# Kernel tuning notes

Measured on AMD Instinct MI355X. Metric: run time of the kernel, lower is better.

The kernel has to match this reference:

```python
import jax, jax.numpy as jnp
import numpy as np


def setup_inputs() -> dict:
    key = jax.random.key(0)
    k1, k2 = jax.random.split(key)
    B, C, H, W = 4, 256, 64, 64
    f_m = jax.random.normal(k1, (B, C, H, W), dtype=jnp.float32)
    f_d = jax.random.normal(k2, (B, C, H, W), dtype=jnp.float32)
    return {"f_m": f_m, "f_d": f_d}


def reference(f_m, f_d):
    B, C, H, W = f_d.shape
    HW = H * W
    f_fuse = f_m + f_d                      # [B, C, H, W]
    f_c = f_fuse.reshape(B, C, HW)          # [B, C, HW]
    # scores[b, n, m] = sum_c f_c[b, c, n] * f_c[b, c, m]
    scores = jnp.einsum('bcn,bcm->bnm', f_c, f_c)   # [B, HW, HW]
    att = jax.nn.softmax(scores, axis=-1)           # softmax over last dim
    f_d_r = f_d.reshape(B, C, HW)                   # [B, C, HW]
    # out[b, c, m] = sum_n f_d_r[b, c, n] * att[b, n, m]
    f_d_att = jnp.einsum('bcn,bnm->bcm', f_d_r, att).reshape(B, C, H, W)
    return f_d_att + f_d
```

## Files before the change

kernel.cpp:

```cpp
#include <hip/hip_runtime.h>
#include <math.h>

#define B_ 4
#define C_ 256
#define N_ 4096
#define LDE 68
#define LDX 72

typedef __attribute__((ext_vector_type(8))) short short8;
typedef __attribute__((ext_vector_type(4))) float f32x4;
typedef __attribute__((ext_vector_type(2))) float f32x2;
typedef __attribute__((ext_vector_type(2))) long long2v;

__device__ inline ushort f2bf(float f) {
    uint u = __float_as_uint(f);
    return (ushort)((u + 0x7fffu + ((u >> 16) & 1u)) >> 16);
}
__device__ inline float bf2f(ushort h) { return __uint_as_float(((uint)h) << 16); }

__device__ inline f32x4 mfma16(short8 a, short8 b, f32x4 c) {
    return __builtin_amdgcn_mfma_f32_16x16x32_bf16(a, b, c, 0, 0, 0);
}
__device__ inline f32x4 mfma8(long a, long b, f32x4 c) {
    return __builtin_amdgcn_mfma_f32_16x16x32_fp8_fp8(a, b, c, 0, 0, 0);
}

__device__ inline size_t xfi16(int b, int nt, int kk2) {
    return (((size_t)(b * 256 + nt)) * 4 + kk2) * 1024;
}
__device__ inline size_t xfi8(int b, int nt, int kk) {
    return (((size_t)(b * 256 + nt)) * 8 + kk) * 512;
}
__device__ inline size_t ffi(int b, int nc, int ct, int k2) {
    return ((((size_t)(b * 64 + nc)) * 16 + ct) * 2 + k2) * 512;
}
__device__ inline size_t eti(int b, int mt, int ng) {
    return (((size_t)(b * 256 + mt)) * 512 + (size_t)ng) * 128;
}
__device__ inline size_t zmi(int b, int nc, int mt) {
    return ((size_t)(b * 64 + nc)) * 256 + mt;
}

__global__ __launch_bounds__(256) void prep_x_kernel(const float* __restrict__ fm,
                                                     const float* __restrict__ fd,
                                                     uchar* __restrict__ xfrag8) {
    __shared__ ushort xl[64][LDX];
    const int b = blockIdx.z, c0 = blockIdx.y * 64, n0 = blockIdx.x * 64;
    const int t = threadIdx.x;
    const int n4 = (t & 15) * 4, cl = t >> 4;
    const size_t base = (size_t)b * C_ * N_;
    #pragma unroll
    for (int p = 0; p < 4; ++p) {
        const int cr = 16 * p + cl;
        const float4 m4 = *(const float4*)(fm + base + (size_t)(c0 + cr) * N_ + n0 + n4);
        const float4 d4 = *(const float4*)(fd + base + (size_t)(c0 + cr) * N_ + n0 + n4);
        ushort4 xo;
        xo.x = f2bf(m4.x + d4.x); xo.y = f2bf(m4.y + d4.y);
        xo.z = f2bf(m4.z + d4.z); xo.w = f2bf(m4.w + d4.w);
        *(ushort4*)(&xl[cr][n4]) = xo;
    }
    __syncthreads();
    const int l = t & 63, tl = t >> 6;
    const int nl = 16 * tl + (l & 15);
    uint dd[4];
    #pragma unroll
    for (int j = 0; j < 2; ++j) {
        const int cb = 32 * j + 8 * (l >> 4);
        float f[8];
        #pragma unroll
        for (int i = 0; i < 8; ++i) f[i] = bf2f(xl[cb + i][nl]);
        int d0 = __builtin_amdgcn_cvt_pk_fp8_f32(f[0], f[1], 0, 0);
        d0 = __builtin_amdgcn_cvt_pk_fp8_f32(f[2], f[3], d0, 1);
        int d1 = __builtin_amdgcn_cvt_pk_fp8_f32(f[4], f[5], 0, 0);
        d1 = __builtin_amdgcn_cvt_pk_fp8_f32(f[6], f[7], d1, 1);
        dd[2 * j] = (uint)d0; dd[2 * j + 1] = (uint)d1;
    }
    uint* dst = (uint*)(xfrag8 + xfi16(b, (n0 >> 4) + tl, c0 >> 6) + (size_t)l * 16);
    dst[0] = dd[0]; dst[1] = dd[1]; dst[2] = dd[2]; dst[3] = dd[3];
}

__global__ __launch_bounds__(256) void dg_kernel(const uchar* __restrict__ xfrag8,
                                                 float* __restrict__ dgall,
                                                 float* __restrict__ rsadd,
                                                 uchar* __restrict__ zmask) {
    const int t = threadIdx.x, lane = t & 63, w = t >> 6;
    const int tid = blockIdx.x * 4 + w;
    const int b = tid >> 8, nt = tid & 255;
    const int l15 = lane & 15, q = lane >> 4;
    long2v af[4];
    #pragma unroll
    for (int kk2 = 0; kk2 < 4; ++kk2)
        af[kk2] = *(const long2v*)(xfrag8 + xfi16(b, nt, kk2) + (size_t)lane * 16);
    f32x4 dacc = {0.f, 0.f, 0.f, 0.f};
    #pragma unroll
    for (int kk2 = 0; kk2 < 4; ++kk2) {
        dacc = mfma8(af[kk2].x, af[kk2].x, dacc);
        dacc = mfma8(af[kk2].y, af[kk2].y, dacc);
    }
    float dvv[4];
    #pragma unroll
    for (int r = 0; r < 4; ++r)
        dvv[r] = __shfl(dacc[r], 20 * q + r, 64);
    if (l15 == 0) {
        #pragma unroll
        for (int r = 0; r < 4; ++r)
            dgall[b * N_ + 16 * nt + 4 * q + r] = dvv[r];
    }
    const int zi = blockIdx.x * 256 + t;
    if (zi < B_ * N_) rsadd[zi] = 0.f;
    zmask[zi] = 0;
}

__global__ __launch_bounds__(512, 2) void lsum_t_kernel(const uchar* __restrict__ xfrag8,
                                                        const float* __restrict__ dgall,
                                                        uchar* __restrict__ E8,
                                                        uchar* __restrict__ zmask,
                                                        float* __restrict__ rsbase,
                                                        float* __restrict__ rsadd) {
    __shared__ float red[8][64];
    __shared__ uchar chl[34];
    __shared__ int cnt_s;
    __shared__ uint zst[34];
    const int bid = blockIdx.x;
    const int b = (bid >> 1) & 3;
    const int n0 = ((((bid >> 3) << 1) | (bid & 1))) * 64;
    const int j = n0 >> 6;
    const int t = threadIdx.x, lane = t & 63, w = t >> 6;
    const int l15 = lane & 15, q = lane >> 4;
    const int g = w >> 2, wm = w & 3;

    if (t == 0) {
        int c = 0;
        chl[c++] = (uchar)j;
        for (int k = 0; k < 64; ++k) {
            if (k == j) continue;
            const bool own = (k > j) ? (((j + k) & 1) == 0) : (((j + k) & 1) == 1);
            if (own) chl[c++] = (uchar)k;
        }
        cnt_s = c;
    }
    if (t < 34) zst[t] = 0u;

    long2v af[4][4];
    #pragma unroll
    for (int ns = 0; ns < 4; ++ns)
        #pragma unroll
        for (int kk2 = 0; kk2 < 4; ++kk2)
            af[ns][kk2] = *(const long2v*)(xfrag8 + xfi16(b, (n0 >> 4) + ns, kk2) + (size_t)lane * 16);

    float dv[4][4];
    #pragma unroll
    for (int ns = 0; ns < 4; ++ns)
        #pragma unroll
        for (int r = 0; r < 4; ++r)
            dv[ns][r] = dgall[b * N_ + n0 + 16 * ns + 4 * q + r];
    float dvmin = dv[0][0];
    #pragma unroll
    for (int ns = 0; ns < 4; ++ns)
        #pragma unroll
        for (int r = 0; r < 4; ++r)
            dvmin = fminf(dvmin, dv[ns][r]);

    __syncthreads();
    const int cnt = cnt_s;

    long2v bn[4];
    float dgm_cur;
    {
        const int mt0 = 4 * (int)chl[g] + wm;
        #pragma unroll
        for (int kk2 = 0; kk2 < 4; ++kk2)
            bn[kk2] = *(const long2v*)(xfrag8 + xfi16(b, mt0, kk2) + (size_t)lane * 16);
        dgm_cur = dgall[b * N_ + 16 * mt0 + l15];
    }
    const size_t ebl = (size_t)l15 * 8 + 4 * (q & 1);
    const int ngb = (n0 >> 3) + (q >> 1);

    float rs[4][4] = {};
    for (int it = 0; it < 17; ++it) {
        const int idx = 2 * it + g;
        const bool valid = idx < cnt;
        const int kc = chl[valid ? idx : 0];
        const int mt = 4 * kc + wm;
        int idxn = 2 * (it + 1) + g; if (idxn >= cnt) idxn = 0;
        const int mtn = 4 * (int)chl[idxn] + wm;

        f32x4 a0 = {0.f,0.f,0.f,0.f}, a1 = {0.f,0.f,0.f,0.f};
        f32x4 a2 = {0.f,0.f,0.f,0.f}, a3 = {0.f,0.f,0.f,0.f};
        __builtin_amdgcn_s_setprio(1);
        #pragma unroll
        for (int kk2 = 0; kk2 < 4; ++kk2) {
            const long2v bc = bn[kk2];
            a0 = mfma8(af[0][kk2].x, bc.x, a0);
            a1 = mfma8(af[1][kk2].x, bc.x, a1);
            a2 = mfma8(af[2][kk2].x, bc.x, a2);
            a3 = mfma8(af[3][kk2].x, bc.x, a3);
            a0 = mfma8(af[0][kk2].y, bc.y, a0);
            a1 = mfma8(af[1][kk2].y, bc.y, a1);
            a2 = mfma8(af[2][kk2].y, bc.y, a2);
            a3 = mfma8(af[3][kk2].y, bc.y, a3);
            bn[kk2] = *(const long2v*)(xfrag8 + xfi16(b, mtn, kk2) + (size_t)lane * 16);
        }
        __builtin_amdgcn_s_setprio(0);
        const float dgm = dgm_cur;
        dgm_cur = dgall[b * N_ + 16 * mtn + l15];

        const float gmax = fmaxf(
            fmaxf(fmaxf(fmaxf(a0[0], a0[1]), fmaxf(a0[2], a0[3])),
                  fmaxf(fmaxf(a1[0], a1[1]), fmaxf(a1[2], a1[3]))),
            fmaxf(fmaxf(fmaxf(a2[0], a2[1]), fmaxf(a2[2], a2[3])),
                  fmaxf(fmaxf(a3[0], a3[1]), fmaxf(a3[2], a3[3]))));
        const bool hot = valid && (__ballot(gmax - fminf(dvmin, dgm) > -30.0f) != 0ULL);
        if (!hot) continue;

        float df[4][4];
#define EDF(AA, NS)                                                    \
        df[NS][0] = AA[0] - dv[NS][0]; df[NS][1] = AA[1] - dv[NS][1];  \
        df[NS][2] = AA[2] - dv[NS][2]; df[NS][3] = AA[3] - dv[NS][3];
        EDF(a0, 0) EDF(a1, 1) EDF(a2, 2) EDF(a3, 3)
#undef EDF
        const float mxA = fmaxf(
            fmaxf(fmaxf(fmaxf(df[0][0], df[0][1]), fmaxf(df[0][2], df[0][3])),
                  fmaxf(fmaxf(df[1][0], df[1][1]), fmaxf(df[1][2], df[1][3]))),
            fmaxf(fmaxf(fmaxf(df[2][0], df[2][1]), fmaxf(df[2][2], df[2][3])),
                  fmaxf(fmaxf(df[3][0], df[3][1]), fmaxf(df[3][2], df[3][3]))));
        const bool nzA = (__ballot(mxA > -30.0f) != 0ULL);
        if (nzA) {
            if (lane == 0) zmask[zmi(b, j, mt)] = 1;
            uint dpk[4];
#define EEXP(NS)                                                                       \
            {                                                                          \
                float e0 = __expf(df[NS][0]), e1 = __expf(df[NS][1]);                  \
                float e2 = __expf(df[NS][2]), e3 = __expf(df[NS][3]);                  \
                rs[NS][0] += e0; rs[NS][1] += e1; rs[NS][2] += e2; rs[NS][3] += e3;    \
                int d = __builtin_amdgcn_cvt_pk_fp8_f32(e0, e1, 0, 0);                 \
                d = __builtin_amdgcn_cvt_pk_fp8_f32(e2, e3, d, 1);                     \
                dpk[NS] = (uint)d;                                                     \
            }
            EEXP(0) EEXP(1) EEXP(2) EEXP(3)
#undef EEXP
            #pragma unroll
            for (int ns = 0; ns < 4; ++ns)
                *(uint*)(E8 + eti(b, mt, ngb + 2 * ns) + ebl) = dpk[ns];
        }
        if (kc != j) {
            float dfB[4][4];
            #pragma unroll
            for (int ns = 0; ns < 4; ++ns) {
                dfB[ns][0] = (ns==0?a0[0]:ns==1?a1[0]:ns==2?a2[0]:a3[0]) - dgm;
                dfB[ns][1] = (ns==0?a0[1]:ns==1?a1[1]:ns==2?a2[1]:a3[1]) - dgm;
                dfB[ns][2] = (ns==0?a0[2]:ns==1?a1[2]:ns==2?a2[2]:a3[2]) - dgm;
                dfB[ns][3] = (ns==0?a0[3]:ns==1?a1[3]:ns==2?a2[3]:a3[3]) - dgm;
            }
            uint bits = 0;
            #pragma unroll
            for (int ns = 0; ns < 4; ++ns) {
                const float m2 = fmaxf(fmaxf(dfB[ns][0], dfB[ns][1]),
                                       fmaxf(dfB[ns][2], dfB[ns][3]));
                if (__ballot(m2 > -30.0f) != 0ULL) bits |= (1u << ns);
            }
            if (bits) {
                if (lane == 0) atomicOr(&zst[idx], bits);
                float cs = 0.f;
                #pragma unroll
                for (int ns = 0; ns < 4; ++ns)
                    #pragma unroll
                    for (int r = 0; r < 4; ++r)
                        cs += __expf(dfB[ns][r]);
                cs += __shfl_xor(cs, 16, 64);
                cs += __shfl_xor(cs, 32, 64);
                if (q == 0) atomicAdd(rsadd + b * N_ + 16 * mt + l15, cs);
            }
        }
    }
    #pragma unroll
    for (int off = 1; off < 16; off <<= 1)
        #pragma unroll
        for (int ns = 0; ns < 4; ++ns)
            #pragma unroll
            for (int r = 0; r < 4; ++r)
                rs[ns][r] += __shfl_xor(rs[ns][r], off, 64);
    if (l15 == 0) {
        #pragma unroll
        for (int ns = 0; ns < 4; ++ns)
            #pragma unroll
            for (int r = 0; r < 4; ++r)
                red[w][16 * ns + 4 * q + r] = rs[ns][r];
    }
    __syncthreads();
    if (t < 64) {
        float s = 0.f;
        #pragma unroll
        for (int ww = 0; ww < 8; ++ww) s += red[ww][t];
        rsbase[b * N_ + n0 + t] = s;
    }
    if (t >= 64 && t < 64 + 33 * 4) {
        const int ii = (t - 64) >> 2, ns = (t - 64) & 3;
        const int idx = ii + 1;
        if (idx < cnt) {
            const int kc = chl[idx];
            if ((zst[idx] >> ns) & 1u) zmask[zmi(b, kc, 4 * j + ns)] = 2;
        }
    }
}

__global__ __launch_bounds__(512, 2) void out_e_kernel(const uchar* __restrict__ E8,
                                                       const uchar* __restrict__ zmask,
                                                       const float* __restrict__ rsbase,
                                                       const float* __restrict__ rsadd,
                                                       const float* __restrict__ dgall,
                                                       const uchar* __restrict__ xfrag8,
                                                       const float* __restrict__ fd32,
                                                       float* __restrict__ outp) {
    __shared__ ushort esc[8][16][66];
    const int bid = blockIdx.x;
    const int b = (bid >> 1) & 3;
    const int m0 = ((((bid >> 3) << 1) | (bid & 1))) * 64;
    const int t = threadIdx.x, lane = t & 63, w = t >> 6;
    const int l15 = lane & 15, q = lane >> 4;
    const size_t fb = (size_t)b * C_ * N_;
    const uchar* mrow = zmask + zmi(b, 0, m0 >> 4);

    f32x4 acc[2][4];
    #pragma unroll
    for (int ct = 0; ct < 2; ++ct)
        #pragma unroll
        for (int mt = 0; mt < 4; ++mt)
            acc[ct][mt] = (f32x4){0.f, 0.f, 0.f, 0.f};

    for (int gg = 0; gg < 8; ++gg) {
        uint mk[8];
        #pragma unroll
        for (int i = 0; i < 8; ++i)
            mk[i] = *(const uint*)(mrow + (size_t)(8 * gg + i) * 256);
        #pragma unroll
        for (int i = 0; i < 8; ++i) {
            const uint mki = mk[i];
            if (mki == 0) continue;
            const int nc = 8 * gg + i;
            const float* rb = rsbase + b * N_ + 64 * nc + 8 * q;
            const float* ra = rsadd + b * N_ + 64 * nc + 8 * q;
            float4 s0[2], s1[2];
            #pragma unroll
            for (int k2 = 0; k2 < 2; ++k2) {
                const float4 b0 = *(const float4*)(rb + 32 * k2);
                const float4 b1 = *(const float4*)(rb + 32 * k2 + 4);
                const float4 a0v = *(const float4*)(ra + 32 * k2);
                const float4 a1v = *(const float4*)(ra + 32 * k2 + 4);
                s0[k2].x = 1.0f / (b0.x + a0v.x); s0[k2].y = 1.0f / (b0.y + a0v.y);
                s0[k2].z = 1.0f / (b0.z + a0v.z); s0[k2].w = 1.0f / (b0.w + a0v.w);
                s1[k2].x = 1.0f / (b1.x + a1v.x); s1[k2].y = 1.0f / (b1.y + a1v.y);
                s1[k2].z = 1.0f / (b1.z + a1v.z); s1[k2].w = 1.0f / (b1.w + a1v.w);
            }
            short8 fn[2][2];
            #pragma unroll
            for (int ct = 0; ct < 2; ++ct) {
                const int c = 32 * w + 16 * ct + l15;
                const float* frow = fd32 + fb + (size_t)c * N_ + 64 * nc + 8 * q;
                #pragma unroll
                for (int k2 = 0; k2 < 2; ++k2) {
                    const float4 fa = *(const float4*)(frow + 32 * k2);
                    const float4 fb4 = *(const float4*)(frow + 32 * k2 + 4);
                    union { ushort us[8]; short8 v; } u;
                    u.us[0] = f2bf(fa.x * s0[k2].x); u.us[1] = f2bf(fa.y * s0[k2].y);
                    u.us[2] = f2bf(fa.z * s0[k2].z); u.us[3] = f2bf(fa.w * s0[k2].w);
                    u.us[4] = f2bf(fb4.x * s1[k2].x); u.us[5] = f2bf(fb4.y * s1[k2].y);
                    u.us[6] = f2bf(fb4.z * s1[k2].z); u.us[7] = f2bf(fb4.w * s1[k2].w);
                    fn[ct][k2] = u.v;
                }
            }
            if ((mki & ~0x01010101u) == 0u) {
                #pragma unroll
                for (int k2 = 0; k2 < 2; ++k2) {
                    #pragma unroll
                    for (int mt = 0; mt < 4; ++mt) {
                        if (((mki >> (8 * mt)) & 0xffu) != 1u) continue;
                        const long e8 = *(const long*)(E8 + eti(b, (m0 >> 4) + mt, 8 * nc + 4 * k2 + q) + (size_t)l15 * 8);
                        const uint lo = (uint)(unsigned long)e8;
                        const uint hi = (uint)((unsigned long)e8 >> 32);
                        const f32x2 f01 = __builtin_amdgcn_cvt_pk_f32_fp8((int)lo, false);
                        const f32x2 f23 = __builtin_amdgcn_cvt_pk_f32_fp8((int)lo, true);
                        const f32x2 f45 = __builtin_amdgcn_cvt_pk_f32_fp8((int)hi, false);
                        const f32x2 f67 = __builtin_amdgcn_cvt_pk_f32_fp8((int)hi, true);
                        union { uint u[4]; short8 v; } be;
                        asm("v_cvt_pk_bf16_f32 %0, %1, %2" : "=v"(be.u[0]) : "v"(f01.x), "v"(f01.y));
                        asm("v_cvt_pk_bf16_f32 %0, %1, %2" : "=v"(be.u[1]) : "v"(f23.x), "v"(f23.y));
                        asm("v_cvt_pk_bf16_f32 %0, %1, %2" : "=v"(be.u[2]) : "v"(f45.x), "v"(f45.y));
                        asm("v_cvt_pk_bf16_f32 %0, %1, %2" : "=v"(be.u[3]) : "v"(f67.x), "v"(f67.y));
                        acc[0][mt] = mfma16(fn[0][k2], be.v, acc[0][mt]);
                        acc[1][mt] = mfma16(fn[1][k2], be.v, acc[1][mt]);
                    }
                }
            } else {
                #pragma unroll
                for (int mt = 0; mt < 4; ++mt) {
                    long2v bmf[4];
                    #pragma unroll
                    for (int kk2 = 0; kk2 < 4; ++kk2)
                        bmf[kk2] = *(const long2v*)(xfrag8 + xfi16(b, (m0 >> 4) + mt, kk2) + (size_t)lane * 16);
                    #pragma unroll
                    for (int nt = 0; nt < 4; ++nt) {
                        long2v anf[4];
                        #pragma unroll
                        for (int kk2 = 0; kk2 < 4; ++kk2)
                            anf[kk2] = *(const long2v*)(xfrag8 + xfi16(b, 4 * nc + nt, kk2) + (size_t)lane * 16);
                        f32x4 sacc = {0.f, 0.f, 0.f, 0.f};
                        #pragma unroll
                        for (int kk2 = 0; kk2 < 4; ++kk2) {
                            sacc = mfma8(anf[kk2].x, bmf[kk2].x, sacc);
                            sacc = mfma8(anf[kk2].y, bmf[kk2].y, sacc);
                        }
                        #pragma unroll
                        for (int r = 0; r < 4; ++r) {
                            const float gv = dgall[b * N_ + 64 * nc + 16 * nt + 4 * q + r];
                            esc[w][l15][16 * nt + 4 * q + r] = f2bf(__expf(sacc[r] - gv));
                        }
                    }
                    #pragma unroll
                    for (int k2 = 0; k2 < 2; ++k2) {
                        const short8 be = *(const short8*)(&esc[w][l15][32 * k2 + 8 * q]);
                        acc[0][mt] = mfma16(fn[0][k2], be, acc[0][mt]);
                        acc[1][mt] = mfma16(fn[1][k2], be, acc[1][mt]);
                    }
                }
            }
        }
    }
    #pragma unroll
    for (int ct = 0; ct < 2; ++ct)
        #pragma unroll
        for (int mt = 0; mt < 4; ++mt)
            #pragma unroll
            for (int r = 0; r < 4; ++r) {
                const int c = 32 * w + 16 * ct + 4 * q + r;
                const int m = m0 + 16 * mt + l15;
                const size_t o = fb + (size_t)c * N_ + m;
                outp[o] = acc[ct][mt][r] + fd32[o];
            }
}

__global__ __launch_bounds__(256) void prep_kernel(const float* __restrict__ fm,
                                                   const float* __restrict__ fd,
                                                   uchar* __restrict__ xfrag8,
                                                   ushort* __restrict__ ffrag) {
    __shared__ ushort xl[64][LDX];
    __shared__ ushort fl[64][LDX];
    const int b = blockIdx.z, c0 = blockIdx.y * 64, n0 = blockIdx.x * 64;
    const int t = threadIdx.x;
    const int n4 = (t & 15) * 4, cl = t >> 4;
    const size_t base = (size_t)b * C_ * N_;
    #pragma unroll
    for (int p = 0; p < 4; ++p) {
        const int cr = 16 * p + cl;
        const float4 m4 = *(const float4*)(fm + base + (size_t)(c0 + cr) * N_ + n0 + n4);
        const float4 d4 = *(const float4*)(fd + base + (size_t)(c0 + cr) * N_ + n0 + n4);
        ushort4 fo;
        fo.x = f2bf(d4.x); fo.y = f2bf(d4.y); fo.z = f2bf(d4.z); fo.w = f2bf(d4.w);
        *(ushort4*)(&fl[cr][n4]) = fo;
        ushort4 xo;
        xo.x = f2bf(m4.x + d4.x); xo.y = f2bf(m4.y + d4.y);
        xo.z = f2bf(m4.z + d4.z); xo.w = f2bf(m4.w + d4.w);
        *(ushort4*)(&xl[cr][n4]) = xo;
    }
    __syncthreads();
    const int l = t & 63, tl = t >> 6;
    {
        const int nl = 16 * tl + (l & 15);
        #pragma unroll
        for (int j = 0; j < 2; ++j) {
            const int kk = (c0 >> 5) + j;
            const int cb = 32 * j + 8 * (l >> 4);
            float f[8];
            #pragma unroll
            for (int i = 0; i < 8; ++i) f[i] = bf2f(xl[cb + i][nl]);
            int d0 = __builtin_amdgcn_cvt_pk_fp8_f32(f[0], f[1], 0, 0);
            d0 = __builtin_amdgcn_cvt_pk_fp8_f32(f[2], f[3], d0, 1);
            int d1 = __builtin_amdgcn_cvt_pk_fp8_f32(f[4], f[5], 0, 0);
            d1 = __builtin_amdgcn_cvt_pk_fp8_f32(f[6], f[7], d1, 1);
            uint* dst = (uint*)(xfrag8 + xfi8(b, (n0 >> 4) + tl, kk) + (size_t)l * 8);
            dst[0] = (uint)d0; dst[1] = (uint)d1;
        }
    }
    {
        const int row = 16 * tl + (l & 15);
        #pragma unroll
        for (int k2 = 0; k2 < 2; ++k2) {
            const int col = 32 * k2 + 8 * (l >> 4);
            const ushort4 a0 = *(const ushort4*)(&fl[row][col]);
            const ushort4 a1 = *(const ushort4*)(&fl[row][col + 4]);
            ushort* dst = ffrag + ffi(b, n0 >> 6, (c0 >> 4) + tl, k2) + l * 8;
            *(ushort4*)(dst) = a0; *(ushort4*)(dst + 4) = a1;
        }
    }
}

__global__ __launch_bounds__(512, 2) void lsum_g_kernel(const uchar* __restrict__ xfrag8,
                                                        float* __restrict__ lg) {
    __shared__ float red[8][64];
    __shared__ float dgl[64];
    const int bid = blockIdx.x;
    const int b = (bid >> 1) & 3;
    const int n0 = ((((bid >> 3) << 1) | (bid & 1))) * 64;
    const int t = threadIdx.x, lane = t & 63, w = t >> 6;
    const int l15 = lane & 15, q = lane >> 4;

    long af[4][8];
    #pragma unroll
    for (int ns = 0; ns < 4; ++ns)
        #pragma unroll
        for (int kk = 0; kk < 8; ++kk)
            af[ns][kk] = *(const long*)(xfrag8 + xfi8(b, (n0 >> 4) + ns, kk) + (size_t)lane * 8);

    float dv[4][4];
    #pragma unroll
    for (int ns = 0; ns < 4; ++ns) {
        f32x4 dacc = {0.f, 0.f, 0.f, 0.f};
        #pragma unroll
        for (int kk = 0; kk < 8; ++kk)
            dacc = mfma8(af[ns][kk], af[ns][kk], dacc);
        #pragma unroll
        for (int r = 0; r < 4; ++r)
            dv[ns][r] = __shfl(dacc[r], 20 * q + r, 64);
    }
    if (w == 0 && l15 == 0) {
        #pragma unroll
        for (int ns = 0; ns < 4; ++ns)
            #pragma unroll
            for (int r = 0; r < 4; ++r)
                dgl[16 * ns + 4 * q + r] = dv[ns][r];
    }

    long bn[8];
    #pragma unroll
    for (int kk = 0; kk < 8; ++kk)
        bn[kk] = *(const long*)(xfrag8 + xfi8(b, w, kk) + (size_t)lane * 8);

    float rs[4][4] = {};
    for (int mc = 0; mc < 32; ++mc) {
        const int mtn = (mc + 1 < 32) ? (mc + 1) * 8 + w : w;
        f32x4 a0 = {0.f,0.f,0.f,0.f}, a1 = {0.f,0.f,0.f,0.f};
        f32x4 a2 = {0.f,0.f,0.f,0.f}, a3 = {0.f,0.f,0.f,0.f};
        #pragma unroll
        for (int kk = 0; kk < 8; ++kk) {
            const long bc = bn[kk];
            a0 = mfma8(af[0][kk], bc, a0);
            a1 = mfma8(af[1][kk], bc, a1);
            a2 = mfma8(af[2][kk], bc, a2);
            a3 = mfma8(af[3][kk], bc, a3);
            bn[kk] = *(const long*)(xfrag8 + xfi8(b, mtn, kk) + (size_t)lane * 8);
        }
        #pragma unroll
        for (int r = 0; r < 4; ++r) {
            rs[0][r] += __expf(a0[r] - dv[0][r]);
            rs[1][r] += __expf(a1[r] - dv[1][r]);
            rs[2][r] += __expf(a2[r] - dv[2][r]);
            rs[3][r] += __expf(a3[r] - dv[3][r]);
        }
    }
    #pragma unroll
    for (int off = 1; off < 16; off <<= 1)
        #pragma unroll
        for (int ns = 0; ns < 4; ++ns)
            #pragma unroll
            for (int r = 0; r < 4; ++r)
                rs[ns][r] += __shfl_xor(rs[ns][r], off, 64);
    if (l15 == 0) {
        #pragma unroll
        for (int ns = 0; ns < 4; ++ns)
            #pragma unroll
            for (int r = 0; r < 4; ++r)
                red[w][16 * ns + 4 * q + r] = rs[ns][r];
    }
    __syncthreads();
    if (t < 64) {
        float s = 0.f;
        #pragma unroll
        for (int ww = 0; ww < 8; ++ww) s += red[ww][t];
        lg[b * N_ + n0 + t] = dgl[t] + __logf(s);
    }
}

__global__ __launch_bounds__(512, 2) void out_g_kernel(const uchar* __restrict__ xfrag8,
                                                       const ushort* __restrict__ ffrag,
                                                       const float* __restrict__ gg,
                                                       const float* __restrict__ fd32,
                                                       float* __restrict__ outp) {
    __shared__ ushort ET[2][64][LDE];
    const int bid = blockIdx.x;
    const int b = (bid >> 1) & 3;
    const int m0 = ((((bid >> 3) << 1) | (bid & 1))) * 64;
    const int t = threadIdx.x, lane = t & 63, w = t >> 6;
    const int l15 = lane & 15, q = lane >> 4;
    const int a = w & 3, h = w >> 2;
    const size_t fb = (size_t)b * C_ * N_;

    long bfr[2][8];
    #pragma unroll
    for (int jt = 0; jt < 2; ++jt)
        #pragma unroll
        for (int kk = 0; kk < 8; ++kk)
            bfr[jt][kk] = *(const long*)(xfrag8 + xfi8(b, (m0 >> 4) + 2 * h + jt, kk) + (size_t)lane * 8);

    f32x4 acc[2][4];
    #pragma unroll
    for (int ct = 0; ct < 2; ++ct)
        #pragma unroll
        for (int mt = 0; mt < 4; ++mt)
            acc[ct][mt] = (f32x4){0.f, 0.f, 0.f, 0.f};

    long an[8];
    #pragma unroll
    for (int kk = 0; kk < 8; ++kk)
        an[kk] = *(const long*)(xfrag8 + xfi8(b, a, kk) + (size_t)lane * 8);
    float gn[4];
    #pragma unroll
    for (int r = 0; r < 4; ++r) gn[r] = gg[b * N_ + 16 * a + 4 * q + r];

    int p = 0;
    for (int n0c = 0; n0c < N_; n0c += 64, p ^= 1) {
        const int nc = n0c >> 6;
        short8 fn[2][2];
        #pragma unroll
        for (int ct = 0; ct < 2; ++ct)
            #pragma unroll
            for (int k2 = 0; k2 < 2; ++k2)
                fn[ct][k2] = *(const short8*)(ffrag + ffi(b, nc, 2 * w + ct, k2) + lane * 8);
        float gv[4];
        #pragma unroll
        for (int r = 0; r < 4; ++r) gv[r] = gn[r];
        const int nx = (n0c + 64 < N_) ? n0c + 64 : 0;
        #pragma unroll
        for (int r = 0; r < 4; ++r) gn[r] = gg[b * N_ + nx + 16 * a + 4 * q + r];

        f32x4 s0 = {0.f, 0.f, 0.f, 0.f}, s1 = {0.f, 0.f, 0.f, 0.f};
        #pragma unroll
        for (int kk = 0; kk < 8; ++kk) {
            s0 = mfma8(an[kk], bfr[0][kk], s0);
            s1 = mfma8(an[kk], bfr[1][kk], s1);
            an[kk] = *(const long*)(xfrag8 + xfi8(b, (nx >> 4) + a, kk) + (size_t)lane * 8);
        }
        ushort4 e0, e1;
        e0.x = f2bf(__expf(s0[0] - gv[0])); e0.y = f2bf(__expf(s0[1] - gv[1]));
        e0.z = f2bf(__expf(s0[2] - gv[2])); e0.w = f2bf(__expf(s0[3] - gv[3]));
        e1.x = f2bf(__expf(s1[0] - gv[0])); e1.y = f2bf(__expf(s1[1] - gv[1]));
        e1.z = f2bf(__expf(s1[2] - gv[2])); e1.w = f2bf(__expf(s1[3] - gv[3]));
        *(ushort4*)(&ET[p][32 * h + l15][16 * a + 4 * q])      = e0;
        *(ushort4*)(&ET[p][32 * h + 16 + l15][16 * a + 4 * q]) = e1;

        asm volatile("s_waitcnt lgkmcnt(0)\n\ts_barrier" ::: "memory");

        #pragma unroll
        for (int k2 = 0; k2 < 2; ++k2) {
            #pragma unroll
            for (int mt = 0; mt < 4; ++mt) {
                const short8 be = *(const short8*)(&ET[p][16 * mt + l15][32 * k2 + 8 * q]);
                acc[0][mt] = mfma16(fn[0][k2], be, acc[0][mt]);
                acc[1][mt] = mfma16(fn[1][k2], be, acc[1][mt]);
            }
        }
    }
    #pragma unroll
    for (int ct = 0; ct < 2; ++ct)
        #pragma unroll
        for (int mt = 0; mt < 4; ++mt)
            #pragma unroll
            for (int r = 0; r < 4; ++r) {
                const int c = 32 * w + 16 * ct + 4 * q + r;
                const int m = m0 + 16 * mt + l15;
                const size_t o = fb + (size_t)c * N_ + m;
                outp[o] = acc[ct][mt][r] + fd32[o];
            }
}

extern "C" void kernel_launch(void* const* d_in, const int* in_sizes, int n_in,
                              void* d_out, int out_size, void* d_ws, size_t ws_size,
                              hipStream_t stream) {
    const float* fm = (const float*)d_in[0];
    const float* fd = (const float*)d_in[1];
    float* outp = (float*)d_out;

    const size_t xb_elts = (size_t)B_ * N_ * C_;
    const size_t e_bytes = (size_t)B_ * N_ * N_;
    const size_t z_bytes = (size_t)B_ * 64 * 256;
    const size_t f_bytes = (size_t)B_ * N_ * 4;
    const size_t need_e  = xb_elts + e_bytes + z_bytes + 3 * f_bytes;
    const size_t need_g  = xb_elts * 3 + f_bytes;

    uchar* xfrag8 = (uchar*)d_ws;

    if (ws_size >= need_e) {
        uchar* E8     = xfrag8 + xb_elts;
        uchar* zmask  = E8 + e_bytes;
        float* rsbase = (float*)(zmask + z_bytes);
        float* rsadd  = rsbase + (size_t)B_ * N_;
        float* dgall  = rsadd + (size_t)B_ * N_;
        prep_x_kernel<<<dim3(N_ / 64, C_ / 64, B_), 256, 0, stream>>>(fm, fd, xfrag8);
        dg_kernel<<<dim3(256), 256, 0, stream>>>(xfrag8, dgall, rsadd, zmask);
        lsum_t_kernel<<<dim3(256), 512, 0, stream>>>(xfrag8, dgall, E8, zmask, rsbase, rsadd);
        out_e_kernel<<<dim3(256), 512, 0, stream>>>(E8, zmask, rsbase, rsadd, dgall, xfrag8, fd, outp);
    } else if (ws_size >= need_g) {
        ushort* ffrag = (ushort*)(xfrag8 + xb_elts);
        float*  lg    = (float*)(xfrag8 + xb_elts * 3);
        prep_kernel<<<dim3(N_ / 64, C_ / 64, B_), 256, 0, stream>>>(fm, fd, xfrag8, ffrag);
        lsum_g_kernel<<<dim3(256), 512, 0, stream>>>(xfrag8, lg);
        out_g_kernel<<<dim3(256), 512, 0, stream>>>(xfrag8, ffrag, lg, fd, outp);
    }
}
```

Measured before the change: 109.1 us.

## Fuse diagonal-block output into row-sum kernel and skip clean output blocks

The row-sum kernel now keeps the diagonal attention tile in shared memory as bf16 and, once the row sums are known, computes that block's output contribution directly (f_d scaled by the inverse row sum, times the diagonal exp tile) and writes out = acc + f_d. The second kernel first checks the zmask for any off-diagonal nonzero tiles or cross-block flags and returns early when the diagonal alone is enough. This targets the common case where the input's strong self-similarity makes the softmax essentially diagonal, avoiding the full E8 output pass. It adds shared memory and work to the first kernel, and relies on out_fix correctly recomputing and overwriting blocks that need off-diagonal terms.

```diff
diff --git a/kernel.cpp b/kernel.cpp
--- a/kernel.cpp
+++ b/kernel.cpp
@@ -111,13 +111,17 @@
     zmask[zi] = 0;
 }
 
-__global__ __launch_bounds__(512, 2) void lsum_t_kernel(const uchar* __restrict__ xfrag8,
-                                                        const float* __restrict__ dgall,
-                                                        uchar* __restrict__ E8,
-                                                        uchar* __restrict__ zmask,
-                                                        float* __restrict__ rsbase,
-                                                        float* __restrict__ rsadd) {
+__global__ __launch_bounds__(512, 2) void fused_kernel(const uchar* __restrict__ xfrag8,
+                                                       const float* __restrict__ dgall,
+                                                       uchar* __restrict__ E8,
+                                                       uchar* __restrict__ zmask,
+                                                       float* __restrict__ rsbase,
+                                                       float* __restrict__ rsadd,
+                                                       const float* __restrict__ fd32,
+                                                       float* __restrict__ outp) {
     __shared__ float red[8][64];
+    __shared__ float sv_l[64];
+    __shared__ ushort ET[64][LDE];
     __shared__ uchar chl[34];
     __shared__ int cnt_s;
     __shared__ uint zst[34];
@@ -128,6 +132,7 @@
     const int t = threadIdx.x, lane = t & 63, w = t >> 6;
     const int l15 = lane & 15, q = lane >> 4;
     const int g = w >> 2, wm = w & 3;
+    const size_t fb = (size_t)b * C_ * N_;
 
     if (t == 0) {
         int c = 0;
@@ -227,6 +232,7 @@
         const bool nzA = (__ballot(mxA > -30.0f) != 0ULL);
         if (nzA) {
             if (lane == 0) zmask[zmi(b, j, mt)] = 1;
+            const bool dia = (kc == j);
             uint dpk[4];
 #define EEXP(NS)                                                                       \
             {                                                                          \
@@ -236,6 +242,12 @@
                 int d = __builtin_amdgcn_cvt_pk_fp8_f32(e0, e1, 0, 0);                 \
                 d = __builtin_amdgcn_cvt_pk_fp8_f32(e2, e3, d, 1);                     \
                 dpk[NS] = (uint)d;                                                     \
+                if (dia) {                                                             \
+                    ushort4 ev;                                                        \
+                    ev.x = f2bf(e0); ev.y = f2bf(e1);                                  \
+                    ev.z = f2bf(e2); ev.w = f2bf(e3);                                  \
+                    *(ushort4*)(&ET[16 * wm + l15][16 * NS + 4 * q]) = ev;             \
+                }                                                                      \
             }
             EEXP(0) EEXP(1) EEXP(2) EEXP(3)
 #undef EEXP
@@ -293,6 +305,7 @@
         #pragma unroll
         for (int ww = 0; ww < 8; ++ww) s += red[ww][t];
         rsbase[b * N_ + n0 + t] = s;
+        sv_l[t] = 1.0f / s;
     }
     if (t >= 64 && t < 64 + 33 * 4) {
         const int ii = (t - 64) >> 2, ns = (t - 64) & 3;
@@ -302,24 +315,86 @@
             if ((zst[idx] >> ns) & 1u) zmask[zmi(b, kc, 4 * j + ns)] = 2;
         }
     }
-}
-
-__global__ __launch_bounds__(512, 2) void out_e_kernel(const uchar* __restrict__ E8,
-                                                       const uchar* __restrict__ zmask,
-                                                       const float* __restrict__ rsbase,
-                                                       const float* __restrict__ rsadd,
-                                                       const float* __restrict__ dgall,
-                                                       const uchar* __restrict__ xfrag8,
-                                                       const float* __restrict__ fd32,
-                                                       float* __restrict__ outp) {
+    __syncthreads();
+
+    {
+        f32x4 pacc[2][4];
+        #pragma unroll
+        for (int ct = 0; ct < 2; ++ct)
+            #pragma unroll
+            for (int mtl = 0; mtl < 4; ++mtl)
+                pacc[ct][mtl] = (f32x4){0.f, 0.f, 0.f, 0.f};
+        short8 pfn[2][2];
+        #pragma unroll
+        for (int ct = 0; ct < 2; ++ct) {
+            const int c = 32 * w + 16 * ct + l15;
+            const float* frow = fd32 + fb + (size_t)c * N_ + 64 * j + 8 * q;
+            #pragma unroll
+            for (int k2 = 0; k2 < 2; ++k2) {
+                const float4 fa = *(const float4*)(frow + 32 * k2);
+                const float4 fb4 = *(const float4*)(frow + 32 * k2 + 4);
+                const int nb = 32 * k2 + 8 * q;
+                union { ushort us[8]; short8 v; } u;
+                u.us[0] = f2bf(fa.x * sv_l[nb + 0]); u.us[1] = f2bf(fa.y * sv_l[nb + 1]);
+                u.us[2] = f2bf(fa.z * sv_l[nb + 2]); u.us[3] = f2bf(fa.w * sv_l[nb + 3]);
+                u.us[4] = f2bf(fb4.x * sv_l[nb + 4]); u.us[5] = f2bf(fb4.y * sv_l[nb + 5]);
+                u.us[6] = f2bf(fb4.z * sv_l[nb + 6]); u.us[7] = f2bf(fb4.w * sv_l[nb + 7]);
+                pfn[ct][k2] = u.v;
+            }
+        }
+        #pragma unroll
+        for (int k2 = 0; k2 < 2; ++k2) {
+            #pragma unroll
+            for (int mtl = 0; mtl < 4; ++mtl) {
+                const short8 be = *(const short8*)(&ET[16 * mtl + l15][32 * k2 + 8 * q]);
+                pacc[0][mtl] = mfma16(pfn[0][k2], be, pacc[0][mtl]);
+                pacc[1][mtl] = mfma16(pfn[1][k2], be, pacc[1][mtl]);
+            }
+        }
+        #pragma unroll
+        for (int ct = 0; ct < 2; ++ct)
+            #pragma unroll
+            for (int mtl = 0; mtl < 4; ++mtl)
+                #pragma unroll
+                for (int r = 0; r < 4; ++r) {
+                    const int c = 32 * w + 16 * ct + 4 * q + r;
+                    const int m = 64 * j + 16 * mtl + l15;
+                    const size_t o = fb + (size_t)c * N_ + m;
+                    outp[o] = pacc[ct][mtl][r] + fd32[o];
+                }
+    }
+}
+
+__global__ __launch_bounds__(512, 2) void out_fix_kernel(const uchar* __restrict__ E8,
+                                                         const uchar* __restrict__ zmask,
+                                                         const float* __restrict__ rsbase,
+                                                         const float* __restrict__ rsadd,
+                                                         const float* __restrict__ dgall,
+                                                         const uchar* __restrict__ xfrag8,
+                                                         const float* __restrict__ fd32,
+                                                         float* __restrict__ outp) {
     __shared__ ushort esc[8][16][66];
+    __shared__ int needfix;
     const int bid = blockIdx.x;
     const int b = (bid >> 1) & 3;
     const int m0 = ((((bid >> 3) << 1) | (bid & 1))) * 64;
+    const int M = m0 >> 6;
     const int t = threadIdx.x, lane = t & 63, w = t >> 6;
     const int l15 = lane & 15, q = lane >> 4;
     const size_t fb = (size_t)b * C_ * N_;
     const uchar* mrow = zmask + zmi(b, 0, m0 >> 4);
+
+    if (t == 0) needfix = 0;
+    __syncthreads();
+    if (t < 64) {
+        const uint ck = *(const uint*)(zmask + zmi(b, t, m0 >> 4));
+        bool bad = (t != M) && (ck != 0u);
+        const uint rk = *(const uint*)(zmask + zmi(b, M, 4 * t));
+        bad |= ((rk & 0x02020202u) != 0u);
+        if (bad) needfix = 1;
+    }
+    __syncthreads();
+    if (needfix == 0) return;
 
     f32x4 acc[2][4];
     #pragma unroll
@@ -696,8 +771,8 @@
         float* dgall  = rsadd + (size_t)B_ * N_;
         prep_x_kernel<<<dim3(N_ / 64, C_ / 64, B_), 256, 0, stream>>>(fm, fd, xfrag8);
         dg_kernel<<<dim3(256), 256, 0, stream>>>(xfrag8, dgall, rsadd, zmask);
-        lsum_t_kernel<<<dim3(256), 512, 0, stream>>>(xfrag8, dgall, E8, zmask, rsbase, rsadd);
-        out_e_kernel<<<dim3(256), 512, 0, stream>>>(E8, zmask, rsbase, rsadd, dgall, xfrag8, fd, outp);
+        fused_kernel<<<dim3(256), 512, 0, stream>>>(xfrag8, dgall, E8, zmask, rsbase, rsadd, fd, outp);
+        out_fix_kernel<<<dim3(256), 512, 0, stream>>>(E8, zmask, rsbase, rsadd, dgall, xfrag8, fd, outp);
     } else if (ws_size >= need_g) {
         ushort* ffrag = (ushort*)(xfrag8 + xb_elts);
         float*  lg    = (float*)(xfrag8 + xb_elts * 3);
```

Result: faster. 103.2 us (-5.4%).
